# Performance work log

Hardware: AMD Instinct MI355X
Metric: run time of the kernel (lower is better)

The kernel has to match this reference:

```python
import jax, jax.numpy as jnp
import numpy as np
import math

N, E = 50000, 800000
DM, H, L = 128, 8, 6
D = DM // H  # per-head dim = 16
FF = 4 * DM
EPS = 1e-5


def _ln(x, g, b):
    mu = jnp.mean(x, axis=-1, keepdims=True)
    var = jnp.mean((x - mu) ** 2, axis=-1, keepdims=True)
    return (x - mu) * jax.lax.rsqrt(var + EPS) * g + b


def setup_inputs() -> dict:
    key = jax.random.key(0)
    ks = jax.random.split(key, 20)
    s = 0.05
    inp = {
        "node_features": jax.random.normal(ks[0], (N, 20), jnp.float32),
        "edge_attr": jax.random.normal(ks[1], (E, 3), jnp.float32),
        "edge_index": jax.random.randint(ks[2], (2, E), 0, N, jnp.int32),
        "emb_W": jax.random.normal(ks[3], (20, DM), jnp.float32) * s,
        "emb_b": jnp.zeros((DM,), jnp.float32),
        "Wq": jax.random.normal(ks[4], (L, DM, DM), jnp.float32) * s,
        "Wk": jax.random.normal(ks[5], (L, DM, DM), jnp.float32) * s,
        "Wv": jax.random.normal(ks[6], (L, DM, DM), jnp.float32) * s,
        "eW1": jax.random.normal(ks[7], (L, 3, D), jnp.float32) * s,
        "eb1": jnp.zeros((L, D), jnp.float32),
        "eW2": jax.random.normal(ks[8], (L, D, DM), jnp.float32) * s,
        "eb2": jnp.zeros((L, DM), jnp.float32),
        "ln_g": jnp.ones((L, DM), jnp.float32),
        "ln_b": jnp.zeros((L, DM), jnp.float32),
        "ff_W1": jax.random.normal(ks[9], (L, DM, FF), jnp.float32) * s,
        "ff_b1": jnp.zeros((L, FF), jnp.float32),
        "ff_W2": jax.random.normal(ks[10], (L, FF, DM), jnp.float32) * s,
        "ff_b2": jnp.zeros((L, DM), jnp.float32),
    }
    return inp


def reference(node_features, edge_attr, emb_W, emb_b, Wq, Wk, Wv,
              eW1, eb1, eW2, eb2, ln_g, ln_b, ff_W1, ff_b1, ff_W2, ff_b2,
              edge_index):
    src = edge_index[0]  # j: message source
    dst = edge_index[1]  # i: message target
    x = node_features @ emb_W + emb_b  # [N, DM]
    scale = 1.0 / math.sqrt(D)
    for l in range(L):
        q = (x @ Wq[l]).reshape(N, H, D)
        k = (x @ Wk[l]).reshape(N, H, D)
        v = (x @ Wv[l]).reshape(N, H, D)
        ee = (jnp.maximum(edge_attr @ eW1[l] + eb1[l], 0.0) @ eW2[l] + eb2[l]).reshape(E, H, D)
        # per-edge attention logits over heads (softmax over head axis, as in source)
        attn = jnp.einsum('ehd,ehd->eh', q[dst], k[src] + ee) * scale
        attn = jax.nn.softmax(attn, axis=1)  # [E, H]
        msg = (attn[..., None] * v[src]).reshape(E, H * D)  # per-head messages, concat heads
        agg = jax.ops.segment_sum(msg, dst, num_segments=N)  # scatter-add
        x = _ln(x + agg, ln_g[l], ln_b[l])
        h = jnp.maximum(x @ ff_W1[l] + ff_b1[l], 0.0) @ ff_W2[l] + ff_b2[l]
        x = _ln(x + h, ln_g[l], ln_b[l])  # same LN params reused, as in source
    return x
```

## Files before the change

kernel.cpp:

```cpp
#include <hip/hip_runtime.h>
#include <cstdint>
#include <cstddef>

#define NN 50000
#define NE 800000
#define NP 50048
#define ROWT 391
#define NBLK 196

typedef unsigned short u16;
typedef _Float16 f16;
typedef _Float16 hf8 __attribute__((ext_vector_type(8)));
typedef float f32x4 __attribute__((ext_vector_type(4)));

union U32 { unsigned u; f16 h[2]; };
union U64 { uint2 v; f16 h[4]; };
union U128 { uint4 v; f16 x[8]; };

__device__ __forceinline__ float b2f(u16 v){ return __uint_as_float((unsigned)v << 16); }
__device__ __forceinline__ u16 f2b(float f){
  unsigned u = __float_as_uint(f);
  return (u16)((u + 0x7fffu + ((u >> 16) & 1u)) >> 16);
}
__device__ __forceinline__ float ldf(const void* p, long i, int f32){
  return f32 ? ((const float*)p)[i] : b2f(((const u16*)p)[i]);
}
__device__ __forceinline__ void gl_lds16(const void* g, void* l){
  __builtin_amdgcn_global_load_lds((const __attribute__((address_space(1))) void*)g,
                                   (__attribute__((address_space(3))) void*)l, 16, 0, 0);
}

__global__ void detect_k(const u16* __restrict__ nf, int* __restrict__ flag)
{
  int mx = 0;
  for (int i = 0; i < 256; ++i) { int e = (nf[i] >> 7) & 0xFF; mx = e > mx ? e : mx; }
  flag[0] = (mx >= 0x90) ? 1 : 0;
}

__global__ void zero_i_k(int* __restrict__ p, int n)
{
  int i = blockIdx.x * 256 + threadIdx.x;
  if (i < n) p[i] = 0;
}

__global__ void conv_k(const void* eW1, const void* eb1, const void* eb2,
                       const void* lng, const void* lnb, const void* fb1, const void* fb2,
                       const void* embB, const void* embW,
                       float* __restrict__ pf, const int* __restrict__ dflag)
{
  int f32 = dflag[0];
  int i = blockIdx.x * 256 + threadIdx.x;
  if (i >= 9216) return;
  const void* p; long off;
  if (i < 288)       { p = eW1;  off = i; }
  else if (i < 384)  { p = eb1;  off = i - 288; }
  else if (i < 1152) { p = eb2;  off = i - 384; }
  else if (i < 1920) { p = lng;  off = i - 1152; }
  else if (i < 2688) { p = lnb;  off = i - 1920; }
  else if (i < 5760) { p = fb1;  off = i - 2688; }
  else if (i < 6528) { p = fb2;  off = i - 5760; }
  else if (i < 6656) { p = embB; off = i - 6528; }
  else               { p = embW; off = i - 6656; }
  pf[i] = ldf(p, off, f32);
}

__global__ void prep_qkve_k(const void* __restrict__ Wq, const void* __restrict__ Wk,
                            const void* __restrict__ Wv, const void* __restrict__ eW2,
                            f16* __restrict__ Wcat, const int* __restrict__ dflag)
{
  int f32 = dflag[0];
  int idx = blockIdx.x * 256 + threadIdx.x;
  int l = idx >> 16;
  int rem = idx & 65535;
  int r = rem >> 7;
  int kk = rem & 127;
  long base = (long)l * 16384;
  float val;
  if (r < 384) {
    const void* W = (r < 128) ? Wq : (r < 256) ? Wk : Wv;
    int n = r & 127;
    val = ldf(W, base + kk * 128 + n, f32);
  } else {
    int n = r - 384, h = n >> 4, j = n & 15;
    long wq = base + kk * 128 + h * 16;
    long e2 = (long)l * 2048 + j * 128 + h * 16;
    float s = 0.f;
    #pragma unroll
    for (int d = 0; d < 16; ++d) s += ldf(Wq, wq + d, f32) * ldf(eW2, e2 + d, f32);
    val = s;
  }
  Wcat[idx] = (f16)val;
}

__global__ void transpose_k(const void* __restrict__ in, f16* __restrict__ out, int R, int C,
                            const int* __restrict__ dflag)
{
  int f32 = dflag[0];
  int idx = blockIdx.x * 256 + threadIdx.x;
  int rc = R * C;
  int l = idx / rc, rem = idx % rc;
  int r = rem / C, c = rem % C;
  out[l * rc + c * R + r] = (f16)ldf(in, idx, f32);
}

__global__ void deg_count_k(const int* __restrict__ eidx, int* __restrict__ deg)
{
  int e = blockIdx.x * 256 + threadIdx.x;
  if (e < NE) atomicAdd(&deg[eidx[NE + e]], 1);
}

__global__ void scan_a(const int* __restrict__ deg, int* __restrict__ bsum)
{
  __shared__ int tmp[256];
  int t = threadIdx.x, i = blockIdx.x * 256 + t;
  int v = (i < NN) ? deg[i] : 0;
  tmp[t] = v; __syncthreads();
  for (int o = 1; o < 256; o <<= 1) {
    int u = (t >= o) ? tmp[t - o] : 0;
    __syncthreads(); tmp[t] += u; __syncthreads();
  }
  if (t == 255) bsum[blockIdx.x] = tmp[255];
}

__global__ void scan_b(const int* __restrict__ bsum, int* __restrict__ boff)
{
  __shared__ int tmp[256];
  int t = threadIdx.x;
  int v = (t < NBLK) ? bsum[t] : 0;
  tmp[t] = v; __syncthreads();
  for (int o = 1; o < 256; o <<= 1) {
    int u = (t >= o) ? tmp[t - o] : 0;
    __syncthreads(); tmp[t] += u; __syncthreads();
  }
  if (t < NBLK) boff[t] = tmp[t] - v;
}

__global__ void scan_c(const int* __restrict__ deg, const int* __restrict__ boff,
                       int* __restrict__ rstart, int* __restrict__ cursor)
{
  __shared__ int tmp[256];
  int t = threadIdx.x, i = blockIdx.x * 256 + t;
  int v = (i < NN) ? deg[i] : 0;
  tmp[t] = v; __syncthreads();
  for (int o = 1; o < 256; o <<= 1) {
    int u = (t >= o) ? tmp[t - o] : 0;
    __syncthreads(); tmp[t] += u; __syncthreads();
  }
  if (i <= NN) {
    int ex = boff[blockIdx.x] + tmp[t] - v;
    rstart[i] = ex;
    if (i < NN) cursor[i] = ex;
  }
}

__global__ void csr_fill_k(const int* __restrict__ eidx, int* __restrict__ cursor,
                           int* __restrict__ csrc, int* __restrict__ cdst,
                           int* __restrict__ ceid)
{
  int e = blockIdx.x * 256 + threadIdx.x;
  if (e >= NE) return;
  int d = eidx[NE + e];
  int slot = atomicAdd(&cursor[d], 1);
  csrc[slot] = eidx[e];
  cdst[slot] = d;
  ceid[slot] = e;
}

__global__ void ea_gather_k(const void* __restrict__ eatt, const int* __restrict__ ceid,
                            f16* __restrict__ ea4, const int* __restrict__ dflag)
{
  int f32 = dflag[0];
  int e = blockIdx.x * 256 + threadIdx.x;
  if (e >= NE) return;
  long id = ceid[e];
  f16* q = ea4 + (size_t)e * 4;
  q[0] = (f16)ldf(eatt, id * 3 + 0, f32);
  q[1] = (f16)ldf(eatt, id * 3 + 1, f32);
  q[2] = (f16)ldf(eatt, id * 3 + 2, f32);
  q[3] = (f16)0.f;
}

__global__ void emb_k(const void* __restrict__ nf, const float* __restrict__ embWf,
                      const float* __restrict__ embBf, float* __restrict__ xf,
                      f16* __restrict__ xh, const int* __restrict__ dflag)
{
  int f32 = dflag[0];
  int idx = blockIdx.x * 256 + threadIdx.x;
  int node = idx >> 7, c = idx & 127;
  float s = 0.f;
  if (node < NN) {
    s = embBf[c];
    long row = (long)node * 20;
    #pragma unroll
    for (int f = 0; f < 20; ++f) s += ldf(nf, row + f, f32) * embWf[f * 128 + c];
  }
  xf[idx] = s;
  xh[idx] = (f16)s;
}

template<int MODE>
__global__ __launch_bounds__(256)
void gemm_k(const f16* __restrict__ A, const f16* __restrict__ Bt, int K,
            f16* __restrict__ o0, f16* __restrict__ o1, f16* __restrict__ o3,
            const float* __restrict__ bias)
{
  __shared__ __align__(16) f16 lA[128 * 64];
  __shared__ __align__(16) f16 lB[128 * 64];
  const int tid = threadIdx.x;
  const int wave = tid >> 6, lane = tid & 63;
  const int wr = wave >> 1, wc = wave & 1;
  const size_t rowBase = (size_t)blockIdx.x * 128;
  const size_t colBase = (size_t)blockIdx.y * 128;
  const int m = lane & 15, q4 = lane >> 4;

  f32x4 zero = {0.f, 0.f, 0.f, 0.f};
  f32x4 acc[4][4];
  #pragma unroll
  for (int i = 0; i < 4; ++i)
    #pragma unroll
    for (int j = 0; j < 4; ++j) acc[i][j] = zero;

  const int sr = lane >> 3, sc = lane & 7;
  const f16* Ap = A + (rowBase + wave * 32 + sr) * (size_t)K + sc * 8;
  const f16* Bp = Bt + (colBase + wave * 32 + sr) * (size_t)K + sc * 8;
  f16* lAp = lA + wave * 2048;
  f16* lBp = lB + wave * 2048;

  for (int k0 = 0; k0 < K; k0 += 64) {
    #pragma unroll
    for (int i = 0; i < 4; ++i) {
      gl_lds16(Ap + k0 + (size_t)(8 * i) * K, lAp + i * 512);
      gl_lds16(Bp + k0 + (size_t)(8 * i) * K, lBp + i * 512);
    }
    __syncthreads();
    hf8 af[2][4], bf[2][4];
    #pragma unroll
    for (int s = 0; s < 2; ++s)
      #pragma unroll
      for (int i = 0; i < 4; ++i) {
        af[s][i] = *(const hf8*)(lA + (wr * 64 + i * 16 + m) * 64 + s * 32 + q4 * 8);
        bf[s][i] = *(const hf8*)(lB + (wc * 64 + i * 16 + m) * 64 + s * 32 + q4 * 8);
      }
    #pragma unroll
    for (int s = 0; s < 2; ++s)
      #pragma unroll
      for (int i = 0; i < 4; ++i)
        #pragma unroll
        for (int j = 0; j < 4; ++j)
          acc[i][j] = __builtin_amdgcn_mfma_f32_16x16x32_f16(af[s][i], bf[s][j], acc[i][j], 0, 0, 0);
    __syncthreads();
  }

  if (MODE == 0) {
    f16* o; size_t ld; int off;
    if (blockIdx.y == 0)      { o = o0; ld = 128; off = 0; }
    else if (blockIdx.y == 1) { o = o1; ld = 256; off = 0; }
    else if (blockIdx.y == 2) { o = o1; ld = 256; off = 128; }
    else                      { o = o3; ld = 128; off = 0; }
    #pragma unroll
    for (int i = 0; i < 4; ++i)
      #pragma unroll
      for (int r = 0; r < 4; ++r) {
        size_t row = rowBase + wr * 64 + i * 16 + q4 * 4 + r;
        #pragma unroll
        for (int j = 0; j < 4; ++j) {
          int col = wc * 64 + j * 16 + m;
          o[row * ld + off + col] = (f16)acc[i][j][r];
        }
      }
  } else if (MODE == 1) {
    #pragma unroll
    for (int j = 0; j < 4; ++j) {
      int colg = (int)colBase + wc * 64 + j * 16 + m;
      float bv = bias[colg];
      #pragma unroll
      for (int i = 0; i < 4; ++i)
        #pragma unroll
        for (int r = 0; r < 4; ++r) {
          size_t row = rowBase + wr * 64 + i * 16 + q4 * 4 + r;
          o0[row * 512 + colg] = (f16)fmaxf(acc[i][j][r] + bv, 0.f);
        }
    }
  } else {
    #pragma unroll
    for (int j = 0; j < 4; ++j) {
      int colg = wc * 64 + j * 16 + m;
      float bv = bias[colg];
      #pragma unroll
      for (int i = 0; i < 4; ++i)
        #pragma unroll
        for (int r = 0; r < 4; ++r) {
          size_t row = rowBase + wr * 64 + i * 16 + q4 * 4 + r;
          o0[row * 128 + colg] = (f16)(acc[i][j][r] + bv);
        }
    }
  }
}

__global__ void pb_k(const f16* __restrict__ qf, const float* __restrict__ eb2f,
                     float* __restrict__ pbt)
{
  int idx = blockIdx.x * 256 + threadIdx.x;
  if (idx >= NN * 8) return;
  int n = idx >> 3, h = idx & 7;
  U128 a, b;
  a.v = *(const uint4*)(qf + (size_t)n * 128 + h * 16);
  b.v = *(const uint4*)(qf + (size_t)n * 128 + h * 16 + 8);
  const float* e = eb2f + h * 16;
  float p = 0.f;
  #pragma unroll
  for (int d = 0; d < 8; ++d) p = fmaf((float)a.x[d], e[d], fmaf((float)b.x[d], e[8 + d], p));
  pbt[idx] = p;
}

__global__ __launch_bounds__(256)
void attn_k(const f16* __restrict__ qf, const f16* __restrict__ kv, const f16* __restrict__ qef,
            const f16* __restrict__ ea4, const int* __restrict__ csrc, const int* __restrict__ cdst,
            const float* __restrict__ pbt, const float* __restrict__ eW1f,
            const float* __restrict__ eb1f, f16* __restrict__ w8)
{
  int e = blockIdx.x * 256 + threadIdx.x;
  if (e >= NE) return;
  int src = csrc[e], dst = cdst[e];
  U64 ue; ue.v = *(const uint2*)(ea4 + (size_t)e * 4);
  float a0 = (float)ue.h[0], a1 = (float)ue.h[1], a2 = (float)ue.h[2];
  float he[16];
  #pragma unroll
  for (int j = 0; j < 16; ++j)
    he[j] = fmaxf(fmaf(a2, eW1f[32 + j], fmaf(a1, eW1f[16 + j], fmaf(a0, eW1f[j], eb1f[j]))), 0.f);
  const uint4* qr = (const uint4*)(qf + (size_t)dst * 128);
  const uint4* kr = (const uint4*)(kv + (size_t)src * 256);
  const uint4* er = (const uint4*)(qef + (size_t)dst * 128);
  float4 pb0 = *(const float4*)(pbt + (size_t)dst * 8);
  float4 pb1 = *(const float4*)(pbt + (size_t)dst * 8 + 4);
  float pbv[8] = { pb0.x, pb0.y, pb0.z, pb0.w, pb1.x, pb1.y, pb1.z, pb1.w };
  float logit[8];
  uint4 qa = qr[0], qb = qr[1], ka = kr[0], kb = kr[1], za = er[0], zb = er[1];
  #pragma unroll
  for (int h = 0; h < 8; ++h) {
    uint4 qa2, qb2, ka2, kb2, za2, zb2;
    if (h < 7) {
      qa2 = qr[2*h+2]; qb2 = qr[2*h+3];
      ka2 = kr[2*h+2]; kb2 = kr[2*h+3];
      za2 = er[2*h+2]; zb2 = er[2*h+3];
    }
    U128 Q0, Q1, K0, K1, E0, E1;
    Q0.v = qa; Q1.v = qb; K0.v = ka; K1.v = kb; E0.v = za; E1.v = zb;
    float p = 0.f;
    #pragma unroll
    for (int d = 0; d < 8; ++d) {
      p = fmaf((float)Q0.x[d], (float)K0.x[d], p);
      p = fmaf((float)Q1.x[d], (float)K1.x[d], p);
      p = fmaf((float)E0.x[d], he[d], p);
      p = fmaf((float)E1.x[d], he[8 + d], p);
    }
    logit[h] = (p + pbv[h]) * 0.25f;
    qa = qa2; qb = qb2; ka = ka2; kb = kb2; za = za2; zb = zb2;
  }
  float mx = logit[0];
  #pragma unroll
  for (int h = 1; h < 8; ++h) mx = fmaxf(mx, logit[h]);
  float se = 0.f, ex[8];
  #pragma unroll
  for (int h = 0; h < 8; ++h) { ex[h] = __expf(logit[h] - mx); se += ex[h]; }
  float inv = 1.f / se;
  U128 W;
  #pragma unroll
  for (int h = 0; h < 8; ++h) W.x[h] = (f16)(ex[h] * inv);
  *(uint4*)(w8 + (size_t)e * 8) = W.v;
}

__global__ void agg_k(const f16* __restrict__ kv, const f16* __restrict__ w8,
                      const int* __restrict__ rstart, const int* __restrict__ csrc,
                      const float* __restrict__ gf, const float* __restrict__ bpf,
                      float* __restrict__ xf, f16* __restrict__ xh)
{
  int wave = threadIdx.x >> 6, lane = threadIdx.x & 63;
  int node = blockIdx.x * 4 + wave;
  if (node >= NN) return;
  int sub = lane >> 4, l = lane & 15;
  int c0 = l << 3;
  int head = l >> 1;
  float acc[8] = {0.f, 0.f, 0.f, 0.f, 0.f, 0.f, 0.f, 0.f};
  int e0 = rstart[node], e1 = rstart[node + 1];
  int e = e0 + sub;
  uint4 vN = {0, 0, 0, 0}; float wN = 0.f;
  if (e < e1) {
    int s = csrc[e];
    vN = *(const uint4*)(kv + (size_t)s * 256 + 128 + c0);
    wN = (float)w8[(size_t)e * 8 + head];
  }
  for (; e < e1; e += 4) {
    uint4 vC = vN; float wC = wN;
    int en = e + 4;
    if (en < e1) {
      int s = csrc[en];
      vN = *(const uint4*)(kv + (size_t)s * 256 + 128 + c0);
      wN = (float)w8[(size_t)en * 8 + head];
    }
    U128 V; V.v = vC;
    #pragma unroll
    for (int i = 0; i < 8; ++i) acc[i] = fmaf(wC, (float)V.x[i], acc[i]);
  }
  #pragma unroll
  for (int i = 0; i < 8; ++i) {
    acc[i] += __shfl_xor(acc[i], 16);
    acc[i] += __shfl_xor(acc[i], 32);
  }
  size_t nb = (size_t)node * 128 + c0;
  float4 x0 = *(const float4*)(xf + nb);
  float4 x1 = *(const float4*)(xf + nb + 4);
  float y[8] = { x0.x + acc[0], x0.y + acc[1], x0.z + acc[2], x0.w + acc[3],
                 x1.x + acc[4], x1.y + acc[5], x1.z + acc[6], x1.w + acc[7] };
  float s1 = 0.f, s2 = 0.f;
  #pragma unroll
  for (int i = 0; i < 8; ++i) { s1 += y[i]; s2 += y[i] * y[i]; }
  #pragma unroll
  for (int o = 1; o < 16; o <<= 1) { s1 += __shfl_xor(s1, o); s2 += __shfl_xor(s2, o); }
  float mu = s1 * 0.0078125f;
  float var = s2 * 0.0078125f - mu * mu;
  float rstd = rsqrtf(var + 1e-5f);
  float ov[8];
  #pragma unroll
  for (int i = 0; i < 8; ++i) ov[i] = (y[i] - mu) * rstd * gf[c0 + i] + bpf[c0 + i];
  if (sub == 0) {
    float4 s0 = { ov[0], ov[1], ov[2], ov[3] };
    float4 s1v = { ov[4], ov[5], ov[6], ov[7] };
    *(float4*)(xf + nb) = s0;
    *(float4*)(xf + nb + 4) = s1v;
    U128 wz;
    #pragma unroll
    for (int i = 0; i < 8; ++i) wz.x[i] = (f16)ov[i];
    *(uint4*)(xh + nb) = wz.v;
  }
}

__global__ void ln_res_k(const f16* __restrict__ add, float* __restrict__ xf,
                         f16* __restrict__ xh, const float* __restrict__ gf,
                         const float* __restrict__ bpf)
{
  int wave = threadIdx.x >> 6, lane = threadIdx.x & 63;
  int node = blockIdx.x * 4 + wave;
  if (node >= NN) return;
  int c0 = lane << 1;
  size_t nb = (size_t)node * 128 + c0;
  U32 ua; ua.u = *(const unsigned*)(add + nb);
  float y0 = xf[nb] + (float)ua.h[0];
  float y1 = xf[nb + 1] + (float)ua.h[1];
  float s1 = y0 + y1, s2 = y0 * y0 + y1 * y1;
  #pragma unroll
  for (int o = 1; o < 64; o <<= 1) { s1 += __shfl_xor(s1, o); s2 += __shfl_xor(s2, o); }
  float mu = s1 * 0.0078125f;
  float var = s2 * 0.0078125f - mu * mu;
  float rstd = rsqrtf(var + 1e-5f);
  float o0v = (y0 - mu) * rstd * gf[c0] + bpf[c0];
  float o1v = (y1 - mu) * rstd * gf[c0 + 1] + bpf[c0 + 1];
  xf[nb] = o0v; xf[nb + 1] = o1v;
  U32 wz; wz.h[0] = (f16)o0v; wz.h[1] = (f16)o1v;
  *(unsigned*)(xh + nb) = wz.u;
}

__global__ void out_k(const float* __restrict__ xf, void* __restrict__ out,
                      const int* __restrict__ dflag)
{
  int f32 = dflag[0];
  int idx = blockIdx.x * 256 + threadIdx.x;
  if (f32) ((float*)out)[idx] = xf[idx];
  else     ((u16*)out)[idx] = f2b(xf[idx]);
}

extern "C" void kernel_launch(void* const* d_in, const int* in_sizes, int n_in,
                              void* d_out, int out_size, void* d_ws, size_t ws_size,
                              hipStream_t stream)
{
  const void* nf   = d_in[0];
  const void* eatt = d_in[1];
  const int*  eidx = (const int*)d_in[2];
  const void* embW = d_in[3];
  const void* embB = d_in[4];
  const void* Wq   = d_in[5];
  const void* Wk   = d_in[6];
  const void* Wv   = d_in[7];
  const void* eW1  = d_in[8];
  const void* eb1  = d_in[9];
  const void* eW2  = d_in[10];
  const void* eb2  = d_in[11];
  const void* lng  = d_in[12];
  const void* lnb  = d_in[13];
  const void* fW1  = d_in[14];
  const void* fb1  = d_in[15];
  const void* fW2  = d_in[16];
  const void* fb2  = d_in[17];

  char* p = (char*)d_ws;
  auto alloc = [&](size_t b) { char* r = p; p += (b + 255) & ~(size_t)255; return r; };
  int* dflag   = (int*)alloc(256);
  float* pf    = (float*)alloc(9216 * 4);
  float* xf    = (float*)alloc((size_t)NP * 128 * 4);
  f16*   xh    = (f16*)  alloc((size_t)NP * 128 * 2);
  int* deg     = (int*)alloc((NN + 1) * 4);
  int* rst     = (int*)alloc((NN + 1) * 4);
  int* cur     = (int*)alloc((size_t)NN * 4);
  int* bsum    = (int*)alloc(NBLK * 4);
  int* boff    = (int*)alloc(NBLK * 4);
  int* csrc    = (int*)alloc((size_t)NE * 4);
  int* cdst    = (int*)alloc((size_t)NE * 4);
  float* pbt   = (float*)alloc((size_t)NN * 8 * 4);
  f16* ea4     = (f16*)alloc((size_t)NE * 4 * 2);
  f16* Wcat    = (f16*)alloc((size_t)6 * 512 * 128 * 2);
  f16* W1t     = (f16*)alloc((size_t)6 * 512 * 128 * 2);
  f16* W2t     = (f16*)alloc((size_t)6 * 128 * 512 * 2);
  char* S    = alloc((size_t)NP * 512 * 2 + (size_t)NP * 128 * 2);
  f16* qf  = (f16*)S;
  f16* qe  = qf + (size_t)NP * 128;
  f16* kv  = qe + (size_t)NP * 128;
  f16* hb  = (f16*)S;
  f16* ffh = hb + (size_t)NP * 512;
  f16* w8  = ffh;
  int* ceid = (int*)S;

  float* eW1f = pf;
  float* eb1f = pf + 288;
  float* eb2f = pf + 384;
  float* lngf = pf + 1152;
  float* lnbf = pf + 1920;
  float* fb1f = pf + 2688;
  float* fb2f = pf + 5760;
  float* embBf = pf + 6528;
  float* embWf = pf + 6656;

  detect_k<<<1, 1, 0, stream>>>((const u16*)nf, dflag);
  conv_k<<<36, 256, 0, stream>>>(eW1, eb1, eb2, lng, lnb, fb1, fb2, embB, embW, pf, dflag);
  prep_qkve_k<<<1536, 256, 0, stream>>>(Wq, Wk, Wv, eW2, Wcat, dflag);
  transpose_k<<<1536, 256, 0, stream>>>(fW1, W1t, 128, 512, dflag);
  transpose_k<<<1536, 256, 0, stream>>>(fW2, W2t, 512, 128, dflag);
  zero_i_k<<<(NN + 256) / 256, 256, 0, stream>>>(deg, NN + 1);
  deg_count_k<<<3125, 256, 0, stream>>>(eidx, deg);
  scan_a<<<NBLK, 256, 0, stream>>>(deg, bsum);
  scan_b<<<1, 256, 0, stream>>>(bsum, boff);
  scan_c<<<NBLK, 256, 0, stream>>>(deg, boff, rst, cur);
  csr_fill_k<<<3125, 256, 0, stream>>>(eidx, cur, csrc, cdst, ceid);
  ea_gather_k<<<3125, 256, 0, stream>>>(eatt, ceid, ea4, dflag);
  emb_k<<<NP * 128 / 256, 256, 0, stream>>>(nf, embWf, embBf, xf, xh, dflag);

  for (int l = 0; l < 6; ++l) {
    gemm_k<0><<<dim3(ROWT, 4), 256, 0, stream>>>(xh, Wcat + (size_t)l * 65536, 128,
                                                 qf, kv, qe, nullptr);
    pb_k<<<(NN * 8 + 255) / 256, 256, 0, stream>>>(qf, eb2f + l * 128, pbt);
    attn_k<<<3125, 256, 0, stream>>>(qf, kv, qe, ea4, csrc, cdst, pbt,
                                     eW1f + l * 48, eb1f + l * 16, w8);
    agg_k<<<12500, 256, 0, stream>>>(kv, w8, rst, csrc,
                                     lngf + l * 128, lnbf + l * 128, xf, xh);
    gemm_k<1><<<dim3(ROWT, 4), 256, 0, stream>>>(xh, W1t + (size_t)l * 65536, 128,
                                                 hb, nullptr, nullptr, fb1f + l * 512);
    gemm_k<2><<<dim3(ROWT, 1), 256, 0, stream>>>(hb, W2t + (size_t)l * 65536, 512,
                                                 ffh, nullptr, nullptr, fb2f + l * 128);
    ln_res_k<<<12500, 256, 0, stream>>>(ffh, xf, xh, lngf + l * 128, lnbf + l * 128);
  }
  out_k<<<25000, 256, 0, stream>>>(xf, d_out, dflag);
}
```

Measured before the change: 1.406 ms.

## Fuse edge attention, softmax and aggregation into one node-centric kernel; stage GEMM epilogue via LDS

Measured after the change: 1.428 ms. About the same (+1.6%).

```diff
diff --git a/kernel.cpp b/kernel.cpp
--- a/kernel.cpp
+++ b/kernel.cpp
@@ -154,15 +154,13 @@
 }
 
 __global__ void csr_fill_k(const int* __restrict__ eidx, int* __restrict__ cursor,
-                           int* __restrict__ csrc, int* __restrict__ cdst,
-                           int* __restrict__ ceid)
+                           int* __restrict__ csrc, int* __restrict__ ceid)
 {
   int e = blockIdx.x * 256 + threadIdx.x;
   if (e >= NE) return;
   int d = eidx[NE + e];
   int slot = atomicAdd(&cursor[d], 1);
   csrc[slot] = eidx[e];
-  cdst[slot] = d;
   ceid[slot] = e;
 }
 
@@ -204,8 +202,9 @@
             f16* __restrict__ o0, f16* __restrict__ o1, f16* __restrict__ o3,
             const float* __restrict__ bias)
 {
-  __shared__ __align__(16) f16 lA[128 * 64];
-  __shared__ __align__(16) f16 lB[128 * 64];
+  __shared__ __align__(16) f16 sh[128 * 136];
+  f16* lA = sh;
+  f16* lB = sh + 8192;
   const int tid = threadIdx.x;
   const int wave = tid >> 6, lane = tid & 63;
   const int wr = wave >> 1, wc = wave & 1;
@@ -247,167 +246,143 @@
       for (int i = 0; i < 4; ++i)
         #pragma unroll
         for (int j = 0; j < 4; ++j)
-          acc[i][j] = __builtin_amdgcn_mfma_f32_16x16x32_f16(af[s][i], bf[s][j], acc[i][j], 0, 0, 0);
+          acc[i][j] = __builtin_amdgcn_mfma_f32_16x16x32_f16(bf[s][j], af[s][i], acc[i][j], 0, 0, 0);
     __syncthreads();
   }
 
+  #pragma unroll
+  for (int i = 0; i < 4; ++i) {
+    int crow = wr * 64 + i * 16 + m;
+    #pragma unroll
+    for (int j = 0; j < 4; ++j) {
+      int ccol = wc * 64 + j * 16 + q4 * 4;
+      float v[4];
+      #pragma unroll
+      for (int r = 0; r < 4; ++r) v[r] = acc[i][j][r];
+      if (MODE == 1) {
+        float4 bv = *(const float4*)(bias + (int)colBase + ccol);
+        v[0] = fmaxf(v[0] + bv.x, 0.f); v[1] = fmaxf(v[1] + bv.y, 0.f);
+        v[2] = fmaxf(v[2] + bv.z, 0.f); v[3] = fmaxf(v[3] + bv.w, 0.f);
+      } else if (MODE == 2) {
+        float4 bv = *(const float4*)(bias + ccol);
+        v[0] += bv.x; v[1] += bv.y; v[2] += bv.z; v[3] += bv.w;
+      }
+      U64 pk;
+      #pragma unroll
+      for (int r = 0; r < 4; ++r) pk.h[r] = (f16)v[r];
+      *(uint2*)(sh + crow * 136 + ccol) = pk.v;
+    }
+  }
+  __syncthreads();
+
+  f16* o; size_t ld; int off;
   if (MODE == 0) {
-    f16* o; size_t ld; int off;
     if (blockIdx.y == 0)      { o = o0; ld = 128; off = 0; }
     else if (blockIdx.y == 1) { o = o1; ld = 256; off = 0; }
     else if (blockIdx.y == 2) { o = o1; ld = 256; off = 128; }
     else                      { o = o3; ld = 128; off = 0; }
-    #pragma unroll
-    for (int i = 0; i < 4; ++i)
-      #pragma unroll
-      for (int r = 0; r < 4; ++r) {
-        size_t row = rowBase + wr * 64 + i * 16 + q4 * 4 + r;
-        #pragma unroll
-        for (int j = 0; j < 4; ++j) {
-          int col = wc * 64 + j * 16 + m;
-          o[row * ld + off + col] = (f16)acc[i][j][r];
-        }
-      }
-  } else if (MODE == 1) {
-    #pragma unroll
-    for (int j = 0; j < 4; ++j) {
-      int colg = (int)colBase + wc * 64 + j * 16 + m;
-      float bv = bias[colg];
-      #pragma unroll
-      for (int i = 0; i < 4; ++i)
-        #pragma unroll
-        for (int r = 0; r < 4; ++r) {
-          size_t row = rowBase + wr * 64 + i * 16 + q4 * 4 + r;
-          o0[row * 512 + colg] = (f16)fmaxf(acc[i][j][r] + bv, 0.f);
-        }
-    }
-  } else {
-    #pragma unroll
-    for (int j = 0; j < 4; ++j) {
-      int colg = wc * 64 + j * 16 + m;
-      float bv = bias[colg];
-      #pragma unroll
-      for (int i = 0; i < 4; ++i)
-        #pragma unroll
-        for (int r = 0; r < 4; ++r) {
-          size_t row = rowBase + wr * 64 + i * 16 + q4 * 4 + r;
-          o0[row * 128 + colg] = (f16)(acc[i][j][r] + bv);
-        }
-    }
-  }
-}
-
-__global__ void pb_k(const f16* __restrict__ qf, const float* __restrict__ eb2f,
-                     float* __restrict__ pbt)
-{
-  int idx = blockIdx.x * 256 + threadIdx.x;
-  if (idx >= NN * 8) return;
-  int n = idx >> 3, h = idx & 7;
-  U128 a, b;
-  a.v = *(const uint4*)(qf + (size_t)n * 128 + h * 16);
-  b.v = *(const uint4*)(qf + (size_t)n * 128 + h * 16 + 8);
-  const float* e = eb2f + h * 16;
-  float p = 0.f;
-  #pragma unroll
-  for (int d = 0; d < 8; ++d) p = fmaf((float)a.x[d], e[d], fmaf((float)b.x[d], e[8 + d], p));
-  pbt[idx] = p;
-}
-
-__global__ __launch_bounds__(256)
-void attn_k(const f16* __restrict__ qf, const f16* __restrict__ kv, const f16* __restrict__ qef,
-            const f16* __restrict__ ea4, const int* __restrict__ csrc, const int* __restrict__ cdst,
-            const float* __restrict__ pbt, const float* __restrict__ eW1f,
-            const float* __restrict__ eb1f, f16* __restrict__ w8)
-{
-  int e = blockIdx.x * 256 + threadIdx.x;
-  if (e >= NE) return;
-  int src = csrc[e], dst = cdst[e];
-  U64 ue; ue.v = *(const uint2*)(ea4 + (size_t)e * 4);
-  float a0 = (float)ue.h[0], a1 = (float)ue.h[1], a2 = (float)ue.h[2];
-  float he[16];
-  #pragma unroll
-  for (int j = 0; j < 16; ++j)
-    he[j] = fmaxf(fmaf(a2, eW1f[32 + j], fmaf(a1, eW1f[16 + j], fmaf(a0, eW1f[j], eb1f[j]))), 0.f);
-  const uint4* qr = (const uint4*)(qf + (size_t)dst * 128);
-  const uint4* kr = (const uint4*)(kv + (size_t)src * 256);
-  const uint4* er = (const uint4*)(qef + (size_t)dst * 128);
-  float4 pb0 = *(const float4*)(pbt + (size_t)dst * 8);
-  float4 pb1 = *(const float4*)(pbt + (size_t)dst * 8 + 4);
-  float pbv[8] = { pb0.x, pb0.y, pb0.z, pb0.w, pb1.x, pb1.y, pb1.z, pb1.w };
-  float logit[8];
-  uint4 qa = qr[0], qb = qr[1], ka = kr[0], kb = kr[1], za = er[0], zb = er[1];
-  #pragma unroll
-  for (int h = 0; h < 8; ++h) {
-    uint4 qa2, qb2, ka2, kb2, za2, zb2;
-    if (h < 7) {
-      qa2 = qr[2*h+2]; qb2 = qr[2*h+3];
-      ka2 = kr[2*h+2]; kb2 = kr[2*h+3];
-      za2 = er[2*h+2]; zb2 = er[2*h+3];
-    }
-    U128 Q0, Q1, K0, K1, E0, E1;
-    Q0.v = qa; Q1.v = qb; K0.v = ka; K1.v = kb; E0.v = za; E1.v = zb;
-    float p = 0.f;
-    #pragma unroll
-    for (int d = 0; d < 8; ++d) {
-      p = fmaf((float)Q0.x[d], (float)K0.x[d], p);
-      p = fmaf((float)Q1.x[d], (float)K1.x[d], p);
-      p = fmaf((float)E0.x[d], he[d], p);
-      p = fmaf((float)E1.x[d], he[8 + d], p);
-    }
-    logit[h] = (p + pbv[h]) * 0.25f;
-    qa = qa2; qb = qb2; ka = ka2; kb = kb2; za = za2; zb = zb2;
-  }
-  float mx = logit[0];
-  #pragma unroll
-  for (int h = 1; h < 8; ++h) mx = fmaxf(mx, logit[h]);
-  float se = 0.f, ex[8];
-  #pragma unroll
-  for (int h = 0; h < 8; ++h) { ex[h] = __expf(logit[h] - mx); se += ex[h]; }
-  float inv = 1.f / se;
-  U128 W;
-  #pragma unroll
-  for (int h = 0; h < 8; ++h) W.x[h] = (f16)(ex[h] * inv);
-  *(uint4*)(w8 + (size_t)e * 8) = W.v;
-}
-
-__global__ void agg_k(const f16* __restrict__ kv, const f16* __restrict__ w8,
-                      const int* __restrict__ rstart, const int* __restrict__ csrc,
-                      const float* __restrict__ gf, const float* __restrict__ bpf,
-                      float* __restrict__ xf, f16* __restrict__ xh)
+  } else if (MODE == 1) { o = o0; ld = 512; off = (int)colBase; }
+  else                  { o = o0; ld = 128; off = 0; }
+  {
+    int row = tid >> 1, half = tid & 1;
+    const f16* srcp = sh + row * 136 + half * 64;
+    f16* dstp = o + (rowBase + row) * ld + off + half * 64;
+    #pragma unroll
+    for (int k = 0; k < 8; ++k)
+      *(uint4*)(dstp + k * 8) = *(const uint4*)(srcp + k * 8);
+  }
+}
+
+__global__ void fuse_k(const f16* __restrict__ qf, const f16* __restrict__ qef,
+                       const f16* __restrict__ kv, const f16* __restrict__ ea4,
+                       const int* __restrict__ rstart, const int* __restrict__ csrc,
+                       const float* __restrict__ eW1f, const float* __restrict__ eb1f,
+                       const float* __restrict__ eb2f,
+                       const float* __restrict__ gf, const float* __restrict__ bpf,
+                       float* __restrict__ xf, f16* __restrict__ xh)
 {
   int wave = threadIdx.x >> 6, lane = threadIdx.x & 63;
   int node = blockIdx.x * 4 + wave;
   if (node >= NN) return;
   int sub = lane >> 4, l = lane & 15;
   int c0 = l << 3;
-  int head = l >> 1;
+  int half = l & 1;
+  size_t nb = (size_t)node * 128 + c0;
+
+  float q[8], z[8];
+  { U128 u; u.v = *(const uint4*)(qf + nb);
+    #pragma unroll
+    for (int i = 0; i < 8; ++i) q[i] = (float)u.x[i];
+    u.v = *(const uint4*)(qef + nb);
+    #pragma unroll
+    for (int i = 0; i < 8; ++i) z[i] = (float)u.x[i]; }
+
+  float pb = 0.f;
+  #pragma unroll
+  for (int i = 0; i < 8; ++i) pb = fmaf(q[i], eb2f[c0 + i], pb);
+  pb += __shfl_xor(pb, 1);
+
+  int j0 = half << 3;
+  float w0[8], w1[8], w2[8], bb[8];
+  #pragma unroll
+  for (int i = 0; i < 8; ++i) {
+    w0[i] = eW1f[j0 + i];
+    w1[i] = eW1f[16 + j0 + i];
+    w2[i] = eW1f[32 + j0 + i];
+    bb[i] = eb1f[j0 + i];
+  }
+
   float acc[8] = {0.f, 0.f, 0.f, 0.f, 0.f, 0.f, 0.f, 0.f};
   int e0 = rstart[node], e1 = rstart[node + 1];
   int e = e0 + sub;
-  uint4 vN = {0, 0, 0, 0}; float wN = 0.f;
+  uint4 kN = {0,0,0,0}, vN = {0,0,0,0};
+  uint2 eaN = {0,0};
   if (e < e1) {
     int s = csrc[e];
-    vN = *(const uint4*)(kv + (size_t)s * 256 + 128 + c0);
-    wN = (float)w8[(size_t)e * 8 + head];
+    const f16* kb = kv + (size_t)s * 256 + c0;
+    kN = *(const uint4*)kb;
+    vN = *(const uint4*)(kb + 128);
+    eaN = *(const uint2*)(ea4 + (size_t)e * 4);
   }
   for (; e < e1; e += 4) {
-    uint4 vC = vN; float wC = wN;
+    uint4 kC = kN, vC = vN; uint2 eaC = eaN;
     int en = e + 4;
     if (en < e1) {
       int s = csrc[en];
-      vN = *(const uint4*)(kv + (size_t)s * 256 + 128 + c0);
-      wN = (float)w8[(size_t)en * 8 + head];
+      const f16* kb = kv + (size_t)s * 256 + c0;
+      kN = *(const uint4*)kb;
+      vN = *(const uint4*)(kb + 128);
+      eaN = *(const uint2*)(ea4 + (size_t)en * 4);
     }
+    U64 ue; ue.v = eaC;
+    float a0 = (float)ue.h[0], a1 = (float)ue.h[1], a2 = (float)ue.h[2];
+    U128 K; K.v = kC;
+    float p = 0.f;
+    #pragma unroll
+    for (int i = 0; i < 8; ++i) {
+      float h = fmaxf(fmaf(a2, w2[i], fmaf(a1, w1[i], fmaf(a0, w0[i], bb[i]))), 0.f);
+      p = fmaf(q[i], (float)K.x[i], fmaf(z[i], h, p));
+    }
+    p += __shfl_xor(p, 1);
+    float logit = (p + pb) * 0.25f;
+    float mx = logit;
+    mx = fmaxf(mx, __shfl_xor(mx, 2));
+    mx = fmaxf(mx, __shfl_xor(mx, 4));
+    mx = fmaxf(mx, __shfl_xor(mx, 8));
+    float ex = __expf(logit - mx);
+    float se = ex;
+    se += __shfl_xor(se, 2); se += __shfl_xor(se, 4); se += __shfl_xor(se, 8);
+    float w = ex / se;
     U128 V; V.v = vC;
     #pragma unroll
-    for (int i = 0; i < 8; ++i) acc[i] = fmaf(wC, (float)V.x[i], acc[i]);
-  }
+    for (int i = 0; i < 8; ++i) acc[i] = fmaf(w, (float)V.x[i], acc[i]);
+  }
+
   #pragma unroll
   for (int i = 0; i < 8; ++i) {
     acc[i] += __shfl_xor(acc[i], 16);
     acc[i] += __shfl_xor(acc[i], 32);
   }
-  size_t nb = (size_t)node * 128 + c0;
   float4 x0 = *(const float4*)(xf + nb);
   float4 x1 = *(const float4*)(xf + nb + 4);
   float y[8] = { x0.x + acc[0], x0.y + acc[1], x0.z + acc[2], x0.w + acc[3],
@@ -504,8 +479,6 @@
   int* bsum    = (int*)alloc(NBLK * 4);
   int* boff    = (int*)alloc(NBLK * 4);
   int* csrc    = (int*)alloc((size_t)NE * 4);
-  int* cdst    = (int*)alloc((size_t)NE * 4);
-  float* pbt   = (float*)alloc((size_t)NN * 8 * 4);
   f16* ea4     = (f16*)alloc((size_t)NE * 4 * 2);
   f16* Wcat    = (f16*)alloc((size_t)6 * 512 * 128 * 2);
   f16* W1t     = (f16*)alloc((size_t)6 * 512 * 128 * 2);
@@ -516,7 +489,6 @@
   f16* kv  = qe + (size_t)NP * 128;
   f16* hb  = (f16*)S;
   f16* ffh = hb + (size_t)NP * 512;
-  f16* w8  = ffh;
   int* ceid = (int*)S;
 
   float* eW1f = pf;
@@ -539,18 +511,16 @@
   scan_a<<<NBLK, 256, 0, stream>>>(deg, bsum);
   scan_b<<<1, 256, 0, stream>>>(bsum, boff);
   scan_c<<<NBLK, 256, 0, stream>>>(deg, boff, rst, cur);
-  csr_fill_k<<<3125, 256, 0, stream>>>(eidx, cur, csrc, cdst, ceid);
+  csr_fill_k<<<3125, 256, 0, stream>>>(eidx, cur, csrc, ceid);
   ea_gather_k<<<3125, 256, 0, stream>>>(eatt, ceid, ea4, dflag);
   emb_k<<<NP * 128 / 256, 256, 0, stream>>>(nf, embWf, embBf, xf, xh, dflag);
 
   for (int l = 0; l < 6; ++l) {
     gemm_k<0><<<dim3(ROWT, 4), 256, 0, stream>>>(xh, Wcat + (size_t)l * 65536, 128,
                                                  qf, kv, qe, nullptr);
-    pb_k<<<(NN * 8 + 255) / 256, 256, 0, stream>>>(qf, eb2f + l * 128, pbt);
-    attn_k<<<3125, 256, 0, stream>>>(qf, kv, qe, ea4, csrc, cdst, pbt,
-                                     eW1f + l * 48, eb1f + l * 16, w8);
-    agg_k<<<12500, 256, 0, stream>>>(kv, w8, rst, csrc,
-                                     lngf + l * 128, lnbf + l * 128, xf, xh);
+    fuse_k<<<12500, 256, 0, stream>>>(qf, qe, kv, ea4, rst, csrc,
+                                      eW1f + l * 48, eb1f + l * 16, eb2f + l * 128,
+                                      lngf + l * 128, lnbf + l * 128, xf, xh);
     gemm_k<1><<<dim3(ROWT, 4), 256, 0, stream>>>(xh, W1t + (size_t)l * 65536, 128,
                                                  hb, nullptr, nullptr, fb1f + l * 512);
     gemm_k<2><<<dim3(ROWT, 1), 256, 0, stream>>>(hb, W2t + (size_t)l * 65536, 512,
```
